# Kernel tuning notes

Measured on AMD Instinct MI355X. Metric: run time of the kernel, lower is better.

## Reference

```python
import jax, jax.numpy as jnp
import numpy as np

B, S, D = 2, 2048, 2048
H, KV, HD = 16, 4, 128
EPS = 1e-6


def setup_inputs() -> dict:
    key = jax.random.key(0)
    ks = jax.random.split(key, 8)
    x = jax.random.normal(ks[0], (B, S, D), dtype=jnp.float32)
    # rope tables: first half cos, second half sin, each [S, HD//2]
    pos = jnp.arange(S, dtype=jnp.float32)[:, None]
    inv_freq = 1.0 / (10000.0 ** (jnp.arange(0, HD, 2, dtype=jnp.float32) / HD))
    ang = pos * inv_freq[None, :]                     # [S, HD//2]
    freqs_cis = jnp.concatenate([jnp.cos(ang), jnp.sin(ang)], axis=-1)  # [S, HD]
    std = 0.02
    Wq = jax.random.normal(ks[1], (H * HD * 2, D), dtype=jnp.float32) * std
    Wk = jax.random.normal(ks[2], (KV * HD, D), dtype=jnp.float32) * std
    Wv = jax.random.normal(ks[3], (KV * HD, D), dtype=jnp.float32) * std
    Wo = jax.random.normal(ks[4], (D, H * HD), dtype=jnp.float32) * std
    q_norm_w = jax.random.normal(ks[5], (HD,), dtype=jnp.float32) * std
    k_norm_w = jax.random.normal(ks[6], (HD,), dtype=jnp.float32) * std
    return {"x": x, "freqs_cis": freqs_cis, "Wq": Wq, "Wk": Wk, "Wv": Wv,
            "Wo": Wo, "q_norm_w": q_norm_w, "k_norm_w": k_norm_w}


def _rmsnorm(x, w):
    xf = x.astype(jnp.float32)
    out = xf * jax.lax.rsqrt(jnp.mean(xf * xf, axis=-1, keepdims=True) + EPS)
    return (out * (1.0 + w.astype(jnp.float32))).astype(x.dtype)


def _rope(t, cos, sin):
    # t: [B,S,h,HD]; cos/sin: [S, HD//2]
    t1, t2 = jnp.split(t, 2, axis=-1)
    c = cos[None, :, None, :]
    s = sin[None, :, None, :]
    return jnp.concatenate([t1 * c - t2 * s, t2 * c + t1 * s], axis=-1)


def reference(x, freqs_cis, Wq, Wk, Wv, Wo, q_norm_w, k_norm_w):
    b, s, _ = x.shape
    q = (x @ Wq.T).reshape(b, s, H, 2 * HD)
    k = (x @ Wk.T).reshape(b, s, KV, HD)
    v = (x @ Wv.T).reshape(b, s, KV, HD)
    q, gate = jnp.split(q, 2, axis=-1)            # each [b,s,H,HD]
    gate = gate.reshape(b, s, H * HD)
    q = _rmsnorm(q, q_norm_w)
    k = _rmsnorm(k, k_norm_w)
    cos, sin = jnp.split(freqs_cis, 2, axis=-1)
    q = _rope(q, cos, sin)
    k = _rope(k, cos, sin)
    # GQA: expand kv heads
    g = H // KV
    k = jnp.repeat(k, g, axis=2)                  # [b,s,H,HD]
    v = jnp.repeat(v, g, axis=2)
    scale = HD ** -0.5
    scores = jnp.einsum('bqhd,bkhd->bhqk', q, k) * scale
    causal = jnp.tril(jnp.ones((s, s), dtype=bool))
    scores = jnp.where(causal[None, None], scores, -jnp.inf)
    probs = jax.nn.softmax(scores, axis=-1)
    attn = jnp.einsum('bhqk,bkhd->bqhd', probs, v).reshape(b, s, H * HD)
    attn = attn * jax.nn.sigmoid(gate)
    return attn @ Wo.T
```

## Files before the change

### kernel.cpp

```cpp
#include <hip/hip_runtime.h>
#include <hip/hip_bf16.h>

#define DEVI __device__ __forceinline__


typedef __attribute__((ext_vector_type(8))) short bfrag;
typedef __attribute__((ext_vector_type(4))) float facc;
typedef __attribute__((ext_vector_type(4))) float f4v;
typedef __attribute__((ext_vector_type(4))) unsigned short us4;

DEVI facc mfma16(bfrag a, bfrag b, facc c) {
  return __builtin_amdgcn_mfma_f32_16x16x32_bf16(a, b, c, 0, 0, 0);
}

DEVI void gl_lds16(const void* g, void* l) {
  __builtin_amdgcn_global_load_lds((__attribute__((address_space(1))) void*)g,
                                   (__attribute__((address_space(3))) void*)l,
                                   16, 0, 0);
}

DEVI int swz128(int a) { return a ^ (((a >> 7) & 7) << 4); }
DEVI int swz256(int a) { return a ^ (((a >> 8) & 7) << 4); }

DEVI unsigned short f2bu(float f) {
  __hip_bfloat16 h = __float2bfloat16(f);
  return *reinterpret_cast<unsigned short*>(&h);
}

__global__ __launch_bounds__(256) void cast_all(const float* __restrict__ x,
                                                const float* __restrict__ Wq,
                                                const float* __restrict__ Wk,
                                                const float* __restrict__ Wv,
                                                const float* __restrict__ Wo,
                                                unsigned short* __restrict__ x_bf,
                                                unsigned short* __restrict__ wqkv,
                                                unsigned short* __restrict__ wo_bf) {
  for (int i = blockIdx.x * 256 + threadIdx.x; i < 5767168; i += gridDim.x * 256) {
    const float* src; unsigned short* dst; int j;
    if (i < 2097152)      { src = x;  dst = x_bf;           j = i; }
    else if (i < 4194304) { src = Wq; dst = wqkv;           j = i - 2097152; }
    else if (i < 4456448) { src = Wk; dst = wqkv + 8388608; j = i - 4194304; }
    else if (i < 4718592) { src = Wv; dst = wqkv + 9437184; j = i - 4456448; }
    else                  { src = Wo; dst = wo_bf;          j = i - 4718592; }
    f4v v = ((const f4v*)src)[j];
    us4 o;
    o[0] = f2bu(v[0]); o[1] = f2bu(v[1]); o[2] = f2bu(v[2]); o[3] = f2bu(v[3]);
    ((us4*)dst)[j] = o;
  }
}

template <typename OUT_T>
__global__ __launch_bounds__(256) void gemm_bt(const __hip_bfloat16* __restrict__ A,
                                               const __hip_bfloat16* __restrict__ Bm,
                                               OUT_T* __restrict__ C,
                                               int M, int N, int K) {
  __shared__ __attribute__((aligned(16))) __hip_bfloat16 As[128 * 64];
  __shared__ __attribute__((aligned(16))) __hip_bfloat16 Bs[128 * 64];
  const int bid = blockIdx.y * gridDim.x + blockIdx.x;
  const int cpx = (gridDim.x * gridDim.y) >> 3;
  const int wg = (bid & 7) * cpx + (bid >> 3);
  const int n0 = (wg % gridDim.x) * 128, m0 = (wg / gridDim.x) * 128;
  const int tid = threadIdx.x, wave = tid >> 6, lane = tid & 63;
  const int lr = lane & 15, lg = lane >> 4;
  const int wr = wave >> 1, wc = wave & 1;

  facc acc[4][4];
#pragma unroll
  for (int m = 0; m < 4; ++m)
#pragma unroll
    for (int n = 0; n < 4; ++n) acc[m][n] = (facc){0.f, 0.f, 0.f, 0.f};

  const char* Ag = (const char*)A;
  const char* Bg = (const char*)Bm;
  const size_t rowb = (size_t)K * 2;

  for (int k0 = 0; k0 < K; k0 += 64) {
#pragma unroll
    for (int i = 0; i < 4; ++i) {
      const int wb = i * 4096 + wave * 1024;
      const int bo = wb + lane * 16;
      const int row = bo >> 7;
      const int kb = swz128(bo) & 127;
      gl_lds16(Ag + (size_t)(m0 + row) * rowb + (size_t)k0 * 2 + kb, (char*)As + wb);
      gl_lds16(Bg + (size_t)(n0 + row) * rowb + (size_t)k0 * 2 + kb, (char*)Bs + wb);
    }
    __syncthreads();
#pragma unroll
    for (int kk = 0; kk < 2; ++kk) {
      bfrag af[4], bf[4];
#pragma unroll
      for (int m = 0; m < 4; ++m)
        af[m] = *(const bfrag*)((const char*)As +
                    ((((wr * 64 + m * 16 + lr) << 7) + kk * 64 + lg * 16) ^ ((lr & 7) << 4)));
#pragma unroll
      for (int n = 0; n < 4; ++n)
        bf[n] = *(const bfrag*)((const char*)Bs +
                    ((((wc * 64 + n * 16 + lr) << 7) + kk * 64 + lg * 16) ^ ((lr & 7) << 4)));
#pragma unroll
      for (int m = 0; m < 4; ++m)
#pragma unroll
        for (int n = 0; n < 4; ++n) acc[m][n] = mfma16(af[m], bf[n], acc[m][n]);
    }
    __syncthreads();
  }

#pragma unroll
  for (int m = 0; m < 4; ++m)
#pragma unroll
    for (int n = 0; n < 4; ++n)
#pragma unroll
      for (int r = 0; r < 4; ++r) {
        const int row = m0 + wr * 64 + m * 16 + lg * 4 + r;
        const int col = n0 + wc * 64 + n * 16 + lr;
        float v = acc[m][n][r];
        if constexpr (sizeof(OUT_T) == 4) C[(size_t)row * N + col] = v;
        else                              C[(size_t)row * N + col] = __float2bfloat16(v);
      }
}

__global__ __launch_bounds__(256) void qnorm_rope(const __hip_bfloat16* __restrict__ qkv,
                                                  const float* __restrict__ w,
                                                  const float* __restrict__ fc,
                                                  __hip_bfloat16* __restrict__ Qb) {
  int item = blockIdx.x * 4 + (threadIdx.x >> 6);
  int lane = threadIdx.x & 63;
  int h = item & 15, bs = item >> 4, s = bs & 2047, b = bs >> 11;
  size_t base = (size_t)bs * 5120 + h * 256;
  float e1 = __bfloat162float(qkv[base + lane]);
  float e2 = __bfloat162float(qkv[base + 64 + lane]);
  float ss = e1 * e1 + e2 * e2;
#pragma unroll
  for (int d = 1; d < 64; d <<= 1) ss += __shfl_xor(ss, d);
  float rr = rsqrtf(ss * (1.0f / 128.0f) + 1e-6f);
  float n1 = e1 * rr * (1.0f + w[lane]);
  float n2 = e2 * rr * (1.0f + w[lane + 64]);
  float cs = fc[s * 128 + lane], sn = fc[s * 128 + 64 + lane];
  size_t ob = ((size_t)((b * 16 + h) * 2048) + s) * 128;
  Qb[ob + lane]      = __float2bfloat16(n1 * cs - n2 * sn);
  Qb[ob + 64 + lane] = __float2bfloat16(n2 * cs + n1 * sn);
}

__global__ __launch_bounds__(256) void knorm_rope(const __hip_bfloat16* __restrict__ qkv,
                                                  const float* __restrict__ w,
                                                  const float* __restrict__ fc,
                                                  __hip_bfloat16* __restrict__ Kb) {
  int item = blockIdx.x * 4 + (threadIdx.x >> 6);
  int lane = threadIdx.x & 63;
  int kv = item & 3, bs = item >> 2, s = bs & 2047, b = bs >> 11;
  size_t base = (size_t)bs * 5120 + 4096 + kv * 128;
  float e1 = __bfloat162float(qkv[base + lane]);
  float e2 = __bfloat162float(qkv[base + 64 + lane]);
  float ss = e1 * e1 + e2 * e2;
#pragma unroll
  for (int d = 1; d < 64; d <<= 1) ss += __shfl_xor(ss, d);
  float rr = rsqrtf(ss * (1.0f / 128.0f) + 1e-6f);
  float n1 = e1 * rr * (1.0f + w[lane]);
  float n2 = e2 * rr * (1.0f + w[lane + 64]);
  float cs = fc[s * 128 + lane], sn = fc[s * 128 + 64 + lane];
  size_t ob = ((size_t)((b * 4 + kv) * 2048) + s) * 128;
  Kb[ob + lane]      = __float2bfloat16(n1 * cs - n2 * sn);
  Kb[ob + 64 + lane] = __float2bfloat16(n2 * cs + n1 * sn);
}

__global__ __launch_bounds__(256) void vtrans(const __hip_bfloat16* __restrict__ qkv,
                                              __hip_bfloat16* __restrict__ vt) {
  __shared__ __hip_bfloat16 tile[64][65];
  int s0 = blockIdx.x * 64, d0 = blockIdx.y * 64, bk = blockIdx.z;
  int b = bk >> 2, kv = bk & 3;
  int tid = threadIdx.x;
#pragma unroll
  for (int i = 0; i < 16; ++i) {
    int e = i * 256 + tid;
    int r = e >> 6, c = e & 63;
    tile[r][c] = qkv[(size_t)(b * 2048 + s0 + r) * 5120 + 4608 + kv * 128 + d0 + c];
  }
  __syncthreads();
#pragma unroll
  for (int i = 0; i < 16; ++i) {
    int e = i * 256 + tid;
    int r = e >> 6, c = e & 63;
    vt[(size_t)(bk * 128 + d0 + r) * 2048 + s0 + c] = tile[c][r];
  }
}

__global__ __launch_bounds__(256) void flash_attn(const __hip_bfloat16* __restrict__ Qb,
                                                  const __hip_bfloat16* __restrict__ Kb,
                                                  const __hip_bfloat16* __restrict__ Vt,
                                                  const __hip_bfloat16* __restrict__ qkv,
                                                  __hip_bfloat16* __restrict__ attn_g) {
  const int n_id = blockIdx.x;
  const int k = n_id >> 8, r = n_id & 255;
  const int qt = (k & 1) ? (31 - (r & 31)) : (r & 31);
  const int hb = (r >> 5) + (k << 3);
  const int h = hb & 15, b = hb >> 4;
  const int kvh = h >> 2;
  const int tid = threadIdx.x, wave = tid >> 6, lane = tid & 63;
  const int lr = lane & 15, lg = lane >> 4;

  __shared__ __attribute__((aligned(16))) __hip_bfloat16 Ks[64 * 128];
  __shared__ __attribute__((aligned(16))) __hip_bfloat16 Vs[128 * 64];
  __shared__ __attribute__((aligned(16))) __hip_bfloat16 Ps[4][16 * 64];

  bfrag qf[4];
  {
    const __hip_bfloat16* Qp =
        Qb + ((size_t)((b * 16 + h) * 2048) + qt * 64 + wave * 16 + lr) * 128;
#pragma unroll
    for (int kk = 0; kk < 4; ++kk) qf[kk] = *(const bfrag*)(Qp + kk * 32 + lg * 8);
  }

  facc o[8];
#pragma unroll
  for (int i = 0; i < 8; ++i) o[i] = (facc){0.f, 0.f, 0.f, 0.f};
  float m_s = -INFINITY;
  float l_s = 0.f;
  const float sc = 0.08838834764831845f;

  const char* Kg0 = (const char*)(Kb + (size_t)((b * 4 + kvh) * 2048) * 128);
  const char* Vg0 = (const char*)(Vt + (size_t)((b * 4 + kvh) * 128) * 2048);
  char* PsW = (char*)&Ps[0][0] + wave * 2048;

  for (int t = 0; t <= qt; ++t) {
#pragma unroll
    for (int i = 0; i < 4; ++i) {
      const int wb = i * 4096 + wave * 1024;
      const int bo = wb + lane * 16;
      gl_lds16(Kg0 + (size_t)t * 16384 + swz256(bo), (char*)Ks + wb);
      const int sa = swz128(bo);
      gl_lds16(Vg0 + (size_t)(bo >> 7) * 4096 + (size_t)t * 128 + (sa & 127),
               (char*)Vs + wb);
    }
    __syncthreads();

    facc st[4];
    __builtin_amdgcn_s_setprio(1);
#pragma unroll
    for (int n = 0; n < 4; ++n) {
      facc a = (facc){0.f, 0.f, 0.f, 0.f};
#pragma unroll
      for (int kk = 0; kk < 4; ++kk) {
        bfrag kf = *(const bfrag*)((const char*)Ks +
                       (((n * 16 + lr) * 256 + kk * 64 + lg * 16) ^ ((lr & 7) << 4)));
        a = mfma16(kf, qf[kk], a);
      }
      st[n] = a;
    }
    __builtin_amdgcn_s_setprio(0);

    const bool diag = (t == qt);
    const int q_local = wave * 16 + lr;
    float pm = -INFINITY;
#pragma unroll
    for (int n = 0; n < 4; ++n)
#pragma unroll
      for (int r2 = 0; r2 < 4; ++r2) {
        float v = st[n][r2] * sc;
        if (diag && (n * 16 + lg * 4 + r2 > q_local)) v = -INFINITY;
        st[n][r2] = v;
        pm = fmaxf(pm, v);
      }
    pm = fmaxf(pm, __shfl_xor(pm, 16));
    pm = fmaxf(pm, __shfl_xor(pm, 32));

    float mn = fmaxf(m_s, pm);
    float alpha = __expf(m_s - mn);
    m_s = mn;

    float lsum = 0.f;
    us4 pw[4];
#pragma unroll
    for (int n = 0; n < 4; ++n)
#pragma unroll
      for (int r2 = 0; r2 < 4; ++r2) {
        float p = __expf(st[n][r2] - m_s);
        lsum += p;
        pw[n][r2] = f2bu(p);
      }
    lsum += __shfl_xor(lsum, 16);
    lsum += __shfl_xor(lsum, 32);
    l_s = l_s * alpha + lsum;

#pragma unroll
    for (int n = 0; n < 4; ++n) {
      const int byte = lr * 128 + n * 32 + lg * 8;
      *(us4*)(PsW + (byte ^ ((lr & 7) << 4))) = pw[n];
    }

    float alpha_acc[4];
#pragma unroll
    for (int r2 = 0; r2 < 4; ++r2) alpha_acc[r2] = __shfl(alpha, lg * 4 + r2);
#pragma unroll
    for (int nn = 0; nn < 8; ++nn)
#pragma unroll
      for (int r2 = 0; r2 < 4; ++r2) o[nn][r2] *= alpha_acc[r2];

    __builtin_amdgcn_s_setprio(1);
#pragma unroll
    for (int kk2 = 0; kk2 < 2; ++kk2) {
      bfrag pa = *(const bfrag*)((const char*)PsW +
                     ((lr * 128 + kk2 * 64 + lg * 16) ^ ((lr & 7) << 4)));
#pragma unroll
      for (int nn = 0; nn < 8; ++nn) {
        bfrag vb = *(const bfrag*)((const char*)Vs +
                       (((nn * 16 + lr) * 128 + kk2 * 64 + lg * 16) ^ ((lr & 7) << 4)));
        o[nn] = mfma16(pa, vb, o[nn]);
      }
    }
    __builtin_amdgcn_s_setprio(0);
    __syncthreads();
  }

  float inv = 1.0f / l_s;
  float inv_acc[4];
#pragma unroll
  for (int r2 = 0; r2 < 4; ++r2) inv_acc[r2] = __shfl(inv, lg * 4 + r2);
  const int q_base = qt * 64 + wave * 16 + lg * 4;
#pragma unroll
  for (int r2 = 0; r2 < 4; ++r2) {
    int q = q_base + r2;
    const __hip_bfloat16* gp = qkv + (size_t)(b * 2048 + q) * 5120 + h * 256 + 128;
    __hip_bfloat16* op = attn_g + (size_t)(b * 2048 + q) * 2048 + h * 128;
#pragma unroll
    for (int nn = 0; nn < 8; ++nn) {
      int d = nn * 16 + lr;
      float g = __bfloat162float(gp[d]);
      float sig = 1.0f / (1.0f + __expf(-g));
      op[d] = __float2bfloat16(o[nn][r2] * inv_acc[r2] * sig);
    }
  }
}

extern "C" void kernel_launch(void* const* d_in, const int* in_sizes, int n_in,
                              void* d_out, int out_size, void* d_ws, size_t ws_size,
                              hipStream_t stream) {
  (void)in_sizes; (void)n_in; (void)out_size; (void)ws_size;
  const float* x  = (const float*)d_in[0];
  const float* fc = (const float*)d_in[1];
  const float* Wq = (const float*)d_in[2];
  const float* Wk = (const float*)d_in[3];
  const float* Wv = (const float*)d_in[4];
  const float* Wo = (const float*)d_in[5];
  const float* qw = (const float*)d_in[6];
  const float* kw = (const float*)d_in[7];
  float* out = (float*)d_out;
  char* ws = (char*)d_ws;

  auto* x_bf   = (__hip_bfloat16*)(ws + 0);
  auto* wqkv   = (__hip_bfloat16*)(ws + 16777216);
  auto* wo_bf  = (__hip_bfloat16*)(ws + 37748736);
  auto* qkvraw = (__hip_bfloat16*)(ws + 46137344);
  auto* vt     = (__hip_bfloat16*)(ws + 88080384);
  auto* attn_g = x_bf;
  auto* Qb     = wqkv;
  auto* Kb     = (__hip_bfloat16*)(ws + 33554432);

  cast_all<<<2048, 256, 0, stream>>>(x, Wq, Wk, Wv, Wo,
                                     (unsigned short*)x_bf,
                                     (unsigned short*)wqkv,
                                     (unsigned short*)wo_bf);

  gemm_bt<__hip_bfloat16><<<dim3(40, 32), 256, 0, stream>>>(x_bf, wqkv, qkvraw, 4096, 5120, 2048);

  qnorm_rope<<<16384, 256, 0, stream>>>(qkvraw, qw, fc, Qb);
  knorm_rope<<<4096, 256, 0, stream>>>(qkvraw, kw, fc, Kb);
  vtrans<<<dim3(32, 2, 8), 256, 0, stream>>>(qkvraw, vt);

  flash_attn<<<1024, 256, 0, stream>>>(Qb, Kb, vt, qkvraw, attn_g);

  gemm_bt<float><<<dim3(16, 32), 256, 0, stream>>>(attn_g, wo_bf, out, 4096, 2048, 2048);
}
```

Baseline: 311.2 us.

## Process two query tiles per flash-attention block to reuse K/V loads

Each flash-attention workgroup now handles 128 query rows (two 64-row sub-tiles) instead of 64. Every K/V tile loaded into LDS then feeds twice as many MFMAs, which halves global K/V traffic and barrier count per query. The grid shrinks from 1024 to 512 blocks and register use roughly doubles for accumulators. The causal mask is now applied on every iteration with relative positions, and the first sub-tile also computes one fully masked extra tile, so it does some wasted work and may run at lower occupancy.

```diff
diff --git a/kernel.cpp b/kernel.cpp
--- a/kernel.cpp
+++ b/kernel.cpp
@@ -190,8 +190,8 @@
                                                   __hip_bfloat16* __restrict__ attn_g) {
   const int n_id = blockIdx.x;
   const int k = n_id >> 8, r = n_id & 255;
-  const int qt = (k & 1) ? (31 - (r & 31)) : (r & 31);
-  const int hb = (r >> 5) + (k << 3);
+  const int qt2 = (k & 1) ? (15 - (r & 15)) : (r & 15);
+  const int hb = (r >> 4) + (k << 4);
   const int h = hb & 15, b = hb >> 4;
   const int kvh = h >> 2;
   const int tid = threadIdx.x, wave = tid >> 6, lane = tid & 63;
@@ -199,28 +199,31 @@
 
   __shared__ __attribute__((aligned(16))) __hip_bfloat16 Ks[64 * 128];
   __shared__ __attribute__((aligned(16))) __hip_bfloat16 Vs[128 * 64];
-  __shared__ __attribute__((aligned(16))) __hip_bfloat16 Ps[4][16 * 64];
-
-  bfrag qf[4];
-  {
+  __shared__ __attribute__((aligned(16))) __hip_bfloat16 Ps[2][4][16 * 64];
+
+  bfrag qf[2][4];
+#pragma unroll
+  for (int s = 0; s < 2; ++s) {
     const __hip_bfloat16* Qp =
-        Qb + ((size_t)((b * 16 + h) * 2048) + qt * 64 + wave * 16 + lr) * 128;
-#pragma unroll
-    for (int kk = 0; kk < 4; ++kk) qf[kk] = *(const bfrag*)(Qp + kk * 32 + lg * 8);
-  }
-
-  facc o[8];
-#pragma unroll
-  for (int i = 0; i < 8; ++i) o[i] = (facc){0.f, 0.f, 0.f, 0.f};
-  float m_s = -INFINITY;
-  float l_s = 0.f;
+        Qb + ((size_t)((b * 16 + h) * 2048) + qt2 * 128 + s * 64 + wave * 16 + lr) * 128;
+#pragma unroll
+    for (int kk = 0; kk < 4; ++kk) qf[s][kk] = *(const bfrag*)(Qp + kk * 32 + lg * 8);
+  }
+
+  facc o[2][8];
+#pragma unroll
+  for (int s = 0; s < 2; ++s)
+#pragma unroll
+    for (int i = 0; i < 8; ++i) o[s][i] = (facc){0.f, 0.f, 0.f, 0.f};
+  float m_s[2] = {-INFINITY, -INFINITY};
+  float l_s[2] = {0.f, 0.f};
   const float sc = 0.08838834764831845f;
 
   const char* Kg0 = (const char*)(Kb + (size_t)((b * 4 + kvh) * 2048) * 128);
   const char* Vg0 = (const char*)(Vt + (size_t)((b * 4 + kvh) * 128) * 2048);
-  char* PsW = (char*)&Ps[0][0] + wave * 2048;
-
-  for (int t = 0; t <= qt; ++t) {
+
+  const int T = 2 * qt2 + 2;
+  for (int t = 0; t < T; ++t) {
 #pragma unroll
     for (int i = 0; i < 4; ++i) {
       const int wb = i * 4096 + wave * 1024;
@@ -232,100 +235,110 @@
     }
     __syncthreads();
 
-    facc st[4];
+    facc st[2][4];
     __builtin_amdgcn_s_setprio(1);
 #pragma unroll
     for (int n = 0; n < 4; ++n) {
-      facc a = (facc){0.f, 0.f, 0.f, 0.f};
+      facc a0 = (facc){0.f, 0.f, 0.f, 0.f};
+      facc a1 = (facc){0.f, 0.f, 0.f, 0.f};
 #pragma unroll
       for (int kk = 0; kk < 4; ++kk) {
         bfrag kf = *(const bfrag*)((const char*)Ks +
                        (((n * 16 + lr) * 256 + kk * 64 + lg * 16) ^ ((lr & 7) << 4)));
-        a = mfma16(kf, qf[kk], a);
-      }
-      st[n] = a;
+        a0 = mfma16(kf, qf[0][kk], a0);
+        a1 = mfma16(kf, qf[1][kk], a1);
+      }
+      st[0][n] = a0; st[1][n] = a1;
     }
     __builtin_amdgcn_s_setprio(0);
 
-    const bool diag = (t == qt);
-    const int q_local = wave * 16 + lr;
-    float pm = -INFINITY;
-#pragma unroll
-    for (int n = 0; n < 4; ++n)
-#pragma unroll
-      for (int r2 = 0; r2 < 4; ++r2) {
-        float v = st[n][r2] * sc;
-        if (diag && (n * 16 + lg * 4 + r2 > q_local)) v = -INFINITY;
-        st[n][r2] = v;
-        pm = fmaxf(pm, v);
-      }
-    pm = fmaxf(pm, __shfl_xor(pm, 16));
-    pm = fmaxf(pm, __shfl_xor(pm, 32));
-
-    float mn = fmaxf(m_s, pm);
-    float alpha = __expf(m_s - mn);
-    m_s = mn;
-
-    float lsum = 0.f;
-    us4 pw[4];
-#pragma unroll
-    for (int n = 0; n < 4; ++n)
-#pragma unroll
-      for (int r2 = 0; r2 < 4; ++r2) {
-        float p = __expf(st[n][r2] - m_s);
-        lsum += p;
-        pw[n][r2] = f2bu(p);
-      }
-    lsum += __shfl_xor(lsum, 16);
-    lsum += __shfl_xor(lsum, 32);
-    l_s = l_s * alpha + lsum;
-
-#pragma unroll
-    for (int n = 0; n < 4; ++n) {
-      const int byte = lr * 128 + n * 32 + lg * 8;
-      *(us4*)(PsW + (byte ^ ((lr & 7) << 4))) = pw[n];
-    }
-
-    float alpha_acc[4];
-#pragma unroll
-    for (int r2 = 0; r2 < 4; ++r2) alpha_acc[r2] = __shfl(alpha, lg * 4 + r2);
-#pragma unroll
-    for (int nn = 0; nn < 8; ++nn)
-#pragma unroll
-      for (int r2 = 0; r2 < 4; ++r2) o[nn][r2] *= alpha_acc[r2];
+#pragma unroll
+    for (int s = 0; s < 2; ++s) {
+      const int q_rel = qt2 * 128 + s * 64 + wave * 16 + lr - t * 64;
+      float pm = -INFINITY;
+#pragma unroll
+      for (int n = 0; n < 4; ++n)
+#pragma unroll
+        for (int r2 = 0; r2 < 4; ++r2) {
+          float v = st[s][n][r2] * sc;
+          if (n * 16 + lg * 4 + r2 > q_rel) v = -INFINITY;
+          st[s][n][r2] = v;
+          pm = fmaxf(pm, v);
+        }
+      pm = fmaxf(pm, __shfl_xor(pm, 16));
+      pm = fmaxf(pm, __shfl_xor(pm, 32));
+
+      float mn = fmaxf(m_s[s], pm);
+      float alpha = __expf(m_s[s] - mn);
+      m_s[s] = mn;
+
+      float lsum = 0.f;
+      us4 pw[4];
+#pragma unroll
+      for (int n = 0; n < 4; ++n)
+#pragma unroll
+        for (int r2 = 0; r2 < 4; ++r2) {
+          float p = __expf(st[s][n][r2] - mn);
+          lsum += p;
+          pw[n][r2] = f2bu(p);
+        }
+      lsum += __shfl_xor(lsum, 16);
+      lsum += __shfl_xor(lsum, 32);
+      l_s[s] = l_s[s] * alpha + lsum;
+
+      char* PsW = (char*)&Ps[s][0][0] + wave * 2048;
+#pragma unroll
+      for (int n = 0; n < 4; ++n) {
+        const int byte = lr * 128 + n * 32 + lg * 8;
+        *(us4*)(PsW + (byte ^ ((lr & 7) << 4))) = pw[n];
+      }
+
+      float aa[4];
+#pragma unroll
+      for (int r2 = 0; r2 < 4; ++r2) aa[r2] = __shfl(alpha, lg * 4 + r2);
+#pragma unroll
+      for (int nn = 0; nn < 8; ++nn)
+#pragma unroll
+        for (int r2 = 0; r2 < 4; ++r2) o[s][nn][r2] *= aa[r2];
+    }
 
     __builtin_amdgcn_s_setprio(1);
 #pragma unroll
     for (int kk2 = 0; kk2 < 2; ++kk2) {
-      bfrag pa = *(const bfrag*)((const char*)PsW +
-                     ((lr * 128 + kk2 * 64 + lg * 16) ^ ((lr & 7) << 4)));
+      const int pb = (lr * 128 + kk2 * 64 + lg * 16) ^ ((lr & 7) << 4);
+      bfrag pa0 = *(const bfrag*)((const char*)&Ps[0][0][0] + wave * 2048 + pb);
+      bfrag pa1 = *(const bfrag*)((const char*)&Ps[1][0][0] + wave * 2048 + pb);
 #pragma unroll
       for (int nn = 0; nn < 8; ++nn) {
         bfrag vb = *(const bfrag*)((const char*)Vs +
                        (((nn * 16 + lr) * 128 + kk2 * 64 + lg * 16) ^ ((lr & 7) << 4)));
-        o[nn] = mfma16(pa, vb, o[nn]);
+        o[0][nn] = mfma16(pa0, vb, o[0][nn]);
+        o[1][nn] = mfma16(pa1, vb, o[1][nn]);
       }
     }
     __builtin_amdgcn_s_setprio(0);
     __syncthreads();
   }
 
-  float inv = 1.0f / l_s;
-  float inv_acc[4];
-#pragma unroll
-  for (int r2 = 0; r2 < 4; ++r2) inv_acc[r2] = __shfl(inv, lg * 4 + r2);
-  const int q_base = qt * 64 + wave * 16 + lg * 4;
-#pragma unroll
-  for (int r2 = 0; r2 < 4; ++r2) {
-    int q = q_base + r2;
-    const __hip_bfloat16* gp = qkv + (size_t)(b * 2048 + q) * 5120 + h * 256 + 128;
-    __hip_bfloat16* op = attn_g + (size_t)(b * 2048 + q) * 2048 + h * 128;
-#pragma unroll
-    for (int nn = 0; nn < 8; ++nn) {
-      int d = nn * 16 + lr;
-      float g = __bfloat162float(gp[d]);
-      float sig = 1.0f / (1.0f + __expf(-g));
-      op[d] = __float2bfloat16(o[nn][r2] * inv_acc[r2] * sig);
+#pragma unroll
+  for (int s = 0; s < 2; ++s) {
+    float inv = 1.0f / l_s[s];
+    float ia[4];
+#pragma unroll
+    for (int r2 = 0; r2 < 4; ++r2) ia[r2] = __shfl(inv, lg * 4 + r2);
+    const int q_base = qt2 * 128 + s * 64 + wave * 16 + lg * 4;
+#pragma unroll
+    for (int r2 = 0; r2 < 4; ++r2) {
+      int q = q_base + r2;
+      const __hip_bfloat16* gp = qkv + (size_t)(b * 2048 + q) * 5120 + h * 256 + 128;
+      __hip_bfloat16* op = attn_g + (size_t)(b * 2048 + q) * 2048 + h * 128;
+#pragma unroll
+      for (int nn = 0; nn < 8; ++nn) {
+        int d = nn * 16 + lr;
+        float g = __bfloat162float(gp[d]);
+        float sig = 1.0f / (1.0f + __expf(-g));
+        op[d] = __float2bfloat16(o[s][nn][r2] * ia[r2] * sig);
+      }
     }
   }
 }
@@ -365,7 +378,7 @@
   knorm_rope<<<4096, 256, 0, stream>>>(qkvraw, kw, fc, Kb);
   vtrans<<<dim3(32, 2, 8), 256, 0, stream>>>(qkvraw, vt);
 
-  flash_attn<<<1024, 256, 0, stream>>>(Qb, Kb, vt, qkvraw, attn_g);
+  flash_attn<<<512, 256, 0, stream>>>(Qb, Kb, vt, qkvraw, attn_g);
 
   gemm_bt<float><<<dim3(16, 32), 256, 0, stream>>>(attn_g, wo_bf, out, 4096, 2048, 2048);
 }
```

Result: slower. 328.4 us (+5.5%).
